# Kernel optimization log

Hardware: AMD Instinct MI355X
Metric: run time of the kernel (lower is better)

The kernel has to match this reference:

```python
import jax, jax.numpy as jnp
import numpy as np

NUM_HEADS = 8


def setup_inputs() -> dict:
    key = jax.random.key(0)
    ks = jax.random.split(key, 9)
    B, C, H, W = 2, 64, 48, 48
    Ck, Cv, Co = 64, 64, 64
    s = lambda fan_in: 1.0 / np.sqrt(fan_in)
    return {
        "x": jax.random.normal(ks[0], (B, C, H, W), jnp.float32),
        "Wq": jax.random.normal(ks[1], (Ck, C), jnp.float32) * s(C),
        "bq": jnp.zeros((Ck,), jnp.float32),
        "Wk": jax.random.normal(ks[2], (Ck, C), jnp.float32) * s(C),
        "bk": jnp.zeros((Ck,), jnp.float32),
        "Wv": jax.random.normal(ks[3], (Cv, C), jnp.float32) * s(C),
        "bv": jnp.zeros((Cv,), jnp.float32),
        "Wo": jax.random.normal(ks[4], (Co, Cv), jnp.float32) * s(Cv),
        "bo": jnp.zeros((Co,), jnp.float32),
    }


def _conv1x1(x, W, b):
    # 1x1 conv == channel matmul: [B,C,H,W] x [O,C] -> [B,O,H,W]
    return jnp.einsum("oc,bchw->bohw", W, x) + b[None, :, None, None]


def reference(x, Wq, bq, Wk, bk, Wv, bv, Wo, bo):
    B, _, H, W_ = x.shape
    nh = NUM_HEADS
    Ck, Cv = Wq.shape[0], Wv.shape[0]
    d = Ck // nh
    L = H * W_

    # NOTE: original torch code scales q in place via a view, so returned q is scaled.
    q = _conv1x1(x, Wq, bq) * (d ** -0.5)
    k = _conv1x1(x, Wk, bk)
    v = _conv1x1(x, Wv, bv)

    qs = q.reshape(B, nh, d, L)          # [B,h,d,Lq]
    ks = k.reshape(B, nh, d, L)          # [B,h,d,Lk]
    vs = v.reshape(B, nh, Cv // nh, L)   # [B,h,dv,Lk]

    logits = jnp.einsum("bhdq,bhdk->bhqk", qs, ks)   # [B,h,Lq,Lk]
    # softmax over the QUERY axis (dim=2), as in the original nn.Softmax(dim=2)
    weights = jax.nn.softmax(logits, axis=2)
    o = jnp.einsum("bhck,bhqk->bhcq", vs, weights)   # [B,h,dv,Lq]

    o = o.reshape(B, Cv, H, W_)
    out = _conv1x1(o, Wo, bo)
    return out, q
```

## Files before the change

kernel.cpp:

```cpp
#include <hip/hip_runtime.h>

#define LL   2304
#define CCH  64
#define NHD  8

static constexpr float QSCALE = 0.35355339059327373f;
static constexpr float LOG2E  = 1.4426950408889634f;

typedef _Float16 half2_t  __attribute__((ext_vector_type(2)));
typedef _Float16 half4_t  __attribute__((ext_vector_type(4)));
typedef _Float16 half8_t  __attribute__((ext_vector_type(8)));
typedef float    float16_t __attribute__((ext_vector_type(16)));

__device__ __forceinline__ half2_t pk_f16(float a, float b) {
    return __builtin_bit_cast(half2_t, __builtin_amdgcn_cvt_pkrtz(a, b));
}


__global__ __launch_bounds__(256) void k_qkv(
    const float* __restrict__ x,
    const float* __restrict__ Wq, const float* __restrict__ bq,
    const float* __restrict__ Wk, const float* __restrict__ bk,
    const float* __restrict__ Wv, const float* __restrict__ bv,
    const float* __restrict__ bo,
    float* __restrict__ qout, float* __restrict__ outp,
    _Float16* __restrict__ Qt, _Float16* __restrict__ Kt, _Float16* __restrict__ Vt)
{
    __shared__ float xs[64][32];
    __shared__ float wsm[64][64];
    const int t   = threadIdx.x;
    const int l0  = blockIdx.x * 32;
    const int b   = blockIdx.y;
    const int mat = blockIdx.z;
    const float* W    = (mat == 0) ? Wq : (mat == 1 ? Wk : Wv);
    const float* bias = (mat == 0) ? bq : (mat == 1 ? bk : bv);
    const float* xb = x + (long)b * CCH * LL;

    if (mat == 0) {
        #pragma unroll
        for (int p = 0; p < 2; ++p) {
            int flat = (p * 256 + t) * 4;
            int co = flat >> 5, l = flat & 31;
            float bv4 = bo[co];
            float4 vv = make_float4(bv4, bv4, bv4, bv4);
            *(float4*)&outp[((long)b * CCH + co) * LL + l0 + l] = vv;
        }
    }

    #pragma unroll
    for (int p = 0; p < 2; ++p) {
        int flat = (p * 256 + t) * 4;
        int c = flat >> 5, l = flat & 31;
        *(float4*)&xs[c][l] = *(const float4*)&xb[(long)c * LL + l0 + l];
    }
    #pragma unroll
    for (int p = 0; p < 4; ++p) {
        int flat = (p * 256 + t) * 4;
        int c = flat >> 6, l = flat & 63;
        *(float4*)&wsm[c][l] = *(const float4*)&W[flat];
    }
    __syncthreads();

    const int l  = t & 31;
    const int cg = t >> 5;
    float acc[8];
    #pragma unroll
    for (int j = 0; j < 8; ++j) acc[j] = 0.f;
    for (int cp = 0; cp < 64; ++cp) {
        float xv = xs[cp][l];
        #pragma unroll
        for (int j = 0; j < 8; ++j) acc[j] = fmaf(wsm[cg * 8 + j][cp], xv, acc[j]);
    }
    long row = (long)(b * NHD + cg) * LL + l0 + l;
    if (mat == 0) {
        half8_t pq;
        #pragma unroll
        for (int j = 0; j < 8; ++j) {
            float qv = (acc[j] + bias[cg * 8 + j]) * QSCALE;
            qout[((long)b * CCH + cg * 8 + j) * LL + l0 + l] = qv;
            pq[j] = (_Float16)(qv * LOG2E);
        }
        *(half8_t*)(Qt + row * 8) = pq;
    } else if (mat == 1) {
        half8_t pk;
        #pragma unroll
        for (int j = 0; j < 8; ++j) pk[j] = (_Float16)(acc[j] + bias[cg * 8 + j]);
        *(half8_t*)(Kt + row * 8) = pk;
    } else {
        half8_t pv;
        #pragma unroll
        for (int j = 0; j < 8; ++j) pv[j] = (_Float16)(acc[j] + bias[cg * 8 + j]);
        *(half8_t*)(Vt + row * 8) = pv;
    }
}

__global__ __launch_bounds__(256) void k_denom(
    const _Float16* __restrict__ Qt, const _Float16* __restrict__ Kt,
    const _Float16* __restrict__ Vt, _Float16* __restrict__ V2)
{
    __shared__ _Float16 lQ[2][256][4];
    __shared__ float Dp[4][32];
    __shared__ float rDs[32];
    const int t    = threadIdx.x;
    const int bh   = blockIdx.y;
    const int k0   = blockIdx.x * 32;
    const int lane = t & 63, w = t >> 6;
    const int half = lane >> 5, l31 = lane & 31;

    half4_t kA = *(const half4_t*)(Kt + ((long)bh * LL + k0 + l31) * 8 + half * 4);

    const float4* qbase = (const float4*)(Qt + (long)bh * LL * 8);
    float4 pre = qbase[t];

    float16_t Dacc = {};
    for (int ch = 0; ch < 9; ++ch) {
        __syncthreads();
        *(float2*)&lQ[0][t][0] = make_float2(pre.x, pre.y);
        *(float2*)&lQ[1][t][0] = make_float2(pre.z, pre.w);
        __syncthreads();
        if (ch + 1 < 9) pre = qbase[(ch + 1) * 256 + t];
        #pragma unroll
        for (int T = 0; T < 2; ++T) {
            half4_t qB = *(const half4_t*)&lQ[half][(2 * w + T) * 32 + l31][0];
            float16_t S = __builtin_amdgcn_mfma_f32_32x32x8f16(kA, qB, (float16_t){}, 0, 0, 0);
            #pragma unroll
            for (int r = 0; r < 16; ++r) Dacc[r] += __builtin_amdgcn_exp2f(S[r]);
        }
    }
    #pragma unroll
    for (int r = 0; r < 16; ++r) {
        float v = Dacc[r];
        v += __shfl_xor(v, 1);  v += __shfl_xor(v, 2);  v += __shfl_xor(v, 4);
        v += __shfl_xor(v, 8);  v += __shfl_xor(v, 16);
        Dacc[r] = v;
    }
    if (l31 == 0) {
        #pragma unroll
        for (int r = 0; r < 16; ++r) {
            int row = (r & 3) + 8 * (r >> 2) + 4 * half;
            Dp[w][row] = Dacc[r];
        }
    }
    __syncthreads();
    if (t < 32) rDs[t] = 256.0f / (Dp[0][t] + Dp[1][t] + Dp[2][t] + Dp[3][t]);
    __syncthreads();
    {
        int kk = t >> 3, c = t & 7;
        float v = (float)Vt[((long)bh * LL + k0 + kk) * 8 + c];
        V2[((long)bh * 8 + c) * LL + k0 + kk] = (_Float16)(v * rDs[kk]);
    }
}

__global__ __launch_bounds__(256, 4) void k_av_out(
    const _Float16* __restrict__ Qt, const _Float16* __restrict__ Kt,
    const _Float16* __restrict__ V2, const float* __restrict__ Wo,
    float* __restrict__ out)
{
    __shared__ _Float16 lK[2][64][4];
    __shared__ _Float16 lVt[8][72];
    __shared__ float WoT[64][68];
    const int t    = threadIdx.x;
    const int bh   = blockIdx.y;
    const int s    = blockIdx.z;
    const int b = bh >> 3, h = bh & 7;
    const int lane = t & 63, w = t >> 6;
    const int half = lane >> 5, l31 = lane & 31;
    const int q0   = blockIdx.x * 128 + w * 32;

    #pragma unroll
    for (int p = 0; p < 4; ++p) {
        int flat = p * 256 + t;
        int co = flat >> 4, cv4 = flat & 15;
        float4 v = *(const float4*)&Wo[co * 64 + cv4 * 4];
        WoT[cv4 * 4 + 0][co] = v.x; WoT[cv4 * 4 + 1][co] = v.y;
        WoT[cv4 * 4 + 2][co] = v.z; WoT[cv4 * 4 + 3][co] = v.w;
    }

    half4_t qB = *(const half4_t*)(Qt + ((long)bh * LL + q0 + l31) * 8 + half * 4);

    const long ks0 = (long)s * 576;
    const float4*    kbase = (const float4*)(Kt + ((long)bh * LL + ks0) * 8);
    const _Float16*  vbase = V2 + (long)bh * 8 * LL + ks0;

    float4 preK, preV;
    if (t < 64) preK = kbase[t];
    else if (t < 128) {
        int c = (t - 64) >> 3, j8 = (t - 64) & 7;
        preV = *(const float4*)(vbase + (long)c * LL + j8 * 8);
    }

    float16_t O = {};
    for (int ch = 0; ch < 9; ++ch) {
        __syncthreads();
        if (t < 64) {
            *(float2*)&lK[0][t][0] = make_float2(preK.x, preK.y);
            *(float2*)&lK[1][t][0] = make_float2(preK.z, preK.w);
        } else if (t < 128) {
            int c = (t - 64) >> 3, j8 = (t - 64) & 7;
            *(float4*)&lVt[c][j8 * 8] = preV;
        }
        __syncthreads();
        if (ch + 1 < 9) {
            if (t < 64) preK = kbase[(ch + 1) * 64 + t];
            else if (t < 128) {
                int c = (t - 64) >> 3, j8 = (t - 64) & 7;
                preV = *(const float4*)(vbase + (long)c * LL + (ch + 1) * 64 + j8 * 8);
            }
        }
        const int cl = l31 & 7;
        #pragma unroll
        for (int T = 0; T < 2; ++T) {
            int kb = T * 32;
            half4_t kA = *(const half4_t*)&lK[half][kb + l31][0];
            float16_t S = __builtin_amdgcn_mfma_f32_32x32x8f16(kA, qB, (float16_t){}, 0, 0, 0);
            #pragma unroll
            for (int g = 0; g < 4; ++g) {
                half2_t p0 = pk_f16(__builtin_amdgcn_exp2f(S[4 * g + 0]),
                                    __builtin_amdgcn_exp2f(S[4 * g + 1]));
                half2_t p1 = pk_f16(__builtin_amdgcn_exp2f(S[4 * g + 2]),
                                    __builtin_amdgcn_exp2f(S[4 * g + 3]));
                half4_t pB = __builtin_shufflevector(p0, p1, 0, 1, 2, 3);
                half4_t vA = *(const half4_t*)&lVt[cl][kb + g * 8 + half * 4];
                O = __builtin_amdgcn_mfma_f32_32x32x8f16(vA, pB, O, 0, 0, 0);
            }
        }
    }

    float ocl[4], och[4];
    #pragma unroll
    for (int r = 0; r < 4; ++r) {
        float mine  = O[r] * (1.0f / 256.0f);
        float other = __shfl_xor(mine, 32);
        ocl[r] = half ? other : mine;
        och[r] = half ? mine  : other;
    }
    float* ob = out + ((long)b * CCH) * LL + q0 + l31;
    #pragma unroll
    for (int g = 0; g < 2; ++g) {
        const int co0 = half * 32 + g * 16;
        float acc2[16];
        #pragma unroll
        for (int j = 0; j < 16; ++j) acc2[j] = 0.f;
        #pragma unroll
        for (int c = 0; c < 8; ++c) {
            float ov = (c < 4) ? ocl[c] : och[c - 4];
            #pragma unroll
            for (int j4 = 0; j4 < 4; ++j4) {
                const float4 wv = *(const float4*)&WoT[h * 8 + c][co0 + j4 * 4];
                acc2[j4 * 4 + 0] = fmaf(wv.x, ov, acc2[j4 * 4 + 0]);
                acc2[j4 * 4 + 1] = fmaf(wv.y, ov, acc2[j4 * 4 + 1]);
                acc2[j4 * 4 + 2] = fmaf(wv.z, ov, acc2[j4 * 4 + 2]);
                acc2[j4 * 4 + 3] = fmaf(wv.w, ov, acc2[j4 * 4 + 3]);
            }
        }
        #pragma unroll
        for (int j = 0; j < 16; ++j)
            atomicAdd(ob + (long)(co0 + j) * LL, acc2[j]);
    }
}

extern "C" void kernel_launch(void* const* d_in, const int* in_sizes, int n_in,
                              void* d_out, int out_size, void* d_ws, size_t ws_size,
                              hipStream_t stream)
{
    const float* x  = (const float*)d_in[0];
    const float* Wq = (const float*)d_in[1];
    const float* bq = (const float*)d_in[2];
    const float* Wk = (const float*)d_in[3];
    const float* bk = (const float*)d_in[4];
    const float* Wv = (const float*)d_in[5];
    const float* bv = (const float*)d_in[6];
    const float* Wo = (const float*)d_in[7];
    const float* bo = (const float*)d_in[8];

    float* out  = (float*)d_out;
    float* qout = out + 294912;

    _Float16* Qt = (_Float16*)d_ws;
    _Float16* Kt = Qt + 294912;
    _Float16* Vt = Kt + 294912;
    _Float16* V2 = Vt + 294912;

    k_qkv   <<<dim3(72, 2, 3),  256, 0, stream>>>(x, Wq, bq, Wk, bk, Wv, bv, bo,
                                                  qout, out, Qt, Kt, Vt);
    k_denom <<<dim3(72, 16),    256, 0, stream>>>(Qt, Kt, Vt, V2);
    k_av_out<<<dim3(18, 16, 4), 256, 0, stream>>>(Qt, Kt, V2, Wo, out);
}
```

Before: 127.3 us.

## Restructure attention-output kernel: all heads per block, 96 queries per wave, fewer atomics

The AV+output kernel now assigns one wave per head within a 512-thread block covering a 96-query tile, staging half of the key split (288 keys) for all heads in shared memory at once. Each wave reuses the staged K/V across three 32-query units. The per-head partial outputs are gathered in shared memory so the output projection sums over all 64 value channels before the atomic adds, cutting atomic traffic by the head count. The cost is much larger shared memory per block, the loss of the register prefetch double-buffering, and only 192 blocks in the grid, which may reduce occupancy and latency hiding.

```diff
diff --git a/kernel.cpp b/kernel.cpp
--- a/kernel.cpp
+++ b/kernel.cpp
@@ -151,111 +151,110 @@
     }
 }
 
-__global__ __launch_bounds__(256, 4) void k_av_out(
+__global__ __launch_bounds__(512) void k_av_out(
     const _Float16* __restrict__ Qt, const _Float16* __restrict__ Kt,
     const _Float16* __restrict__ V2, const float* __restrict__ Wo,
     float* __restrict__ out)
 {
-    __shared__ _Float16 lK[2][64][4];
-    __shared__ _Float16 lVt[8][72];
-    __shared__ float WoT[64][68];
+    __shared__ _Float16 lK[8][2][288][4];
+    __shared__ _Float16 lV[8][8][296];
+    __shared__ float    WoT[64][68];
+    __shared__ float    Os[64][100];
     const int t    = threadIdx.x;
-    const int bh   = blockIdx.y;
+    const int qb   = blockIdx.x;
+    const int b    = blockIdx.y;
     const int s    = blockIdx.z;
-    const int b = bh >> 3, h = bh & 7;
-    const int lane = t & 63, w = t >> 6;
+    const int lane = t & 63, h = t >> 6;
     const int half = lane >> 5, l31 = lane & 31;
-    const int q0   = blockIdx.x * 128 + w * 32;
-
-    #pragma unroll
-    for (int p = 0; p < 4; ++p) {
-        int flat = p * 256 + t;
+    const int cl   = l31 & 7;
+    const int bh   = b * NHD + h;
+
+    #pragma unroll
+    for (int p = 0; p < 2; ++p) {
+        int flat = p * 512 + t;
         int co = flat >> 4, cv4 = flat & 15;
         float4 v = *(const float4*)&Wo[co * 64 + cv4 * 4];
         WoT[cv4 * 4 + 0][co] = v.x; WoT[cv4 * 4 + 1][co] = v.y;
         WoT[cv4 * 4 + 2][co] = v.z; WoT[cv4 * 4 + 3][co] = v.w;
     }
 
-    half4_t qB = *(const half4_t*)(Qt + ((long)bh * LL + q0 + l31) * 8 + half * 4);
-
-    const long ks0 = (long)s * 576;
-    const float4*    kbase = (const float4*)(Kt + ((long)bh * LL + ks0) * 8);
-    const _Float16*  vbase = V2 + (long)bh * 8 * LL + ks0;
-
-    float4 preK, preV;
-    if (t < 64) preK = kbase[t];
-    else if (t < 128) {
-        int c = (t - 64) >> 3, j8 = (t - 64) & 7;
-        preV = *(const float4*)(vbase + (long)c * LL + j8 * 8);
-    }
-
-    float16_t O = {};
-    for (int ch = 0; ch < 9; ++ch) {
-        __syncthreads();
-        if (t < 64) {
-            *(float2*)&lK[0][t][0] = make_float2(preK.x, preK.y);
-            *(float2*)&lK[1][t][0] = make_float2(preK.z, preK.w);
-        } else if (t < 128) {
-            int c = (t - 64) >> 3, j8 = (t - 64) & 7;
-            *(float4*)&lVt[c][j8 * 8] = preV;
-        }
-        __syncthreads();
-        if (ch + 1 < 9) {
-            if (t < 64) preK = kbase[(ch + 1) * 64 + t];
-            else if (t < 128) {
-                int c = (t - 64) >> 3, j8 = (t - 64) & 7;
-                preV = *(const float4*)(vbase + (long)c * LL + (ch + 1) * 64 + j8 * 8);
-            }
-        }
-        const int cl = l31 & 7;
-        #pragma unroll
-        for (int T = 0; T < 2; ++T) {
-            int kb = T * 32;
-            half4_t kA = *(const half4_t*)&lK[half][kb + l31][0];
-            float16_t S = __builtin_amdgcn_mfma_f32_32x32x8f16(kA, qB, (float16_t){}, 0, 0, 0);
-            #pragma unroll
-            for (int g = 0; g < 4; ++g) {
-                half2_t p0 = pk_f16(__builtin_amdgcn_exp2f(S[4 * g + 0]),
-                                    __builtin_amdgcn_exp2f(S[4 * g + 1]));
-                half2_t p1 = pk_f16(__builtin_amdgcn_exp2f(S[4 * g + 2]),
-                                    __builtin_amdgcn_exp2f(S[4 * g + 3]));
-                half4_t pB = __builtin_shufflevector(p0, p1, 0, 1, 2, 3);
-                half4_t vA = *(const half4_t*)&lVt[cl][kb + g * 8 + half * 4];
-                O = __builtin_amdgcn_mfma_f32_32x32x8f16(vA, pB, O, 0, 0, 0);
-            }
-        }
-    }
-
-    float ocl[4], och[4];
+    const long qrow = (long)bh * LL + qb * 96 + l31;
+    half4_t qB0 = *(const half4_t*)(Qt + (qrow +  0) * 8 + half * 4);
+    half4_t qB1 = *(const half4_t*)(Qt + (qrow + 32) * 8 + half * 4);
+    half4_t qB2 = *(const half4_t*)(Qt + (qrow + 64) * 8 + half * 4);
+
+    float16_t O0 = {}, O1 = {}, O2 = {};
+
+    #define UNIT_STEP(Oacc, qBu)                                               \
+        _Pragma("unroll")                                                      \
+        for (int k32 = 0; k32 < 9; ++k32) {                                    \
+            const int kb = k32 * 32;                                           \
+            half4_t kA = *(const half4_t*)&lK[h][half][kb + l31][0];           \
+            float16_t S = __builtin_amdgcn_mfma_f32_32x32x8f16(kA, qBu, (float16_t){}, 0, 0, 0); \
+            _Pragma("unroll")                                                  \
+            for (int g = 0; g < 4; ++g) {                                      \
+                half2_t p0 = pk_f16(__builtin_amdgcn_exp2f(S[4*g+0]),          \
+                                    __builtin_amdgcn_exp2f(S[4*g+1]));         \
+                half2_t p1 = pk_f16(__builtin_amdgcn_exp2f(S[4*g+2]),          \
+                                    __builtin_amdgcn_exp2f(S[4*g+3]));         \
+                half4_t pB = __builtin_shufflevector(p0, p1, 0, 1, 2, 3);      \
+                half4_t vA = *(const half4_t*)&lV[h][cl][kb + g*8 + half*4];   \
+                Oacc = __builtin_amdgcn_mfma_f32_32x32x8f16(vA, pB, Oacc, 0, 0, 0); \
+            }                                                                  \
+        }
+
+    for (int kh = 0; kh < 2; ++kh) {
+        const long ksb = (long)s * 576 + kh * 288;
+        __syncthreads();
+        for (int i = t; i < 2304; i += 512) {
+            int hi = i / 288, row = i - hi * 288;
+            float4 kv = *(const float4*)&Kt[((long)(b * NHD + hi) * LL + ksb + row) * 8];
+            *(float2*)&lK[hi][0][row][0] = make_float2(kv.x, kv.y);
+            *(float2*)&lK[hi][1][row][0] = make_float2(kv.z, kv.w);
+        }
+        for (int i = t; i < 2304; i += 512) {
+            int r = i / 36, j = i - r * 36;
+            int hi = r >> 3, c = r & 7;
+            *(float4*)&lV[hi][c][j * 8] =
+                *(const float4*)&V2[((long)(b * NHD + hi) * NHD + c) * LL + ksb + j * 8];
+        }
+        __syncthreads();
+        UNIT_STEP(O0, qB0)
+        UNIT_STEP(O1, qB1)
+        UNIT_STEP(O2, qB2)
+    }
+    #undef UNIT_STEP
+
     #pragma unroll
     for (int r = 0; r < 4; ++r) {
-        float mine  = O[r] * (1.0f / 256.0f);
-        float other = __shfl_xor(mine, 32);
-        ocl[r] = half ? other : mine;
-        och[r] = half ? mine  : other;
-    }
-    float* ob = out + ((long)b * CCH) * LL + q0 + l31;
-    #pragma unroll
-    for (int g = 0; g < 2; ++g) {
-        const int co0 = half * 32 + g * 16;
-        float acc2[16];
-        #pragma unroll
-        for (int j = 0; j < 16; ++j) acc2[j] = 0.f;
-        #pragma unroll
-        for (int c = 0; c < 8; ++c) {
-            float ov = (c < 4) ? ocl[c] : och[c - 4];
+        const int c = r + 4 * half;
+        Os[h * 8 + c][ 0 + l31] = O0[r] * (1.0f / 256.0f);
+        Os[h * 8 + c][32 + l31] = O1[r] * (1.0f / 256.0f);
+        Os[h * 8 + c][64 + l31] = O2[r] * (1.0f / 256.0f);
+    }
+    __syncthreads();
+
+    if (t < 384) {
+        const int q   = t % 96;
+        const int cog = t / 96;
+        float acc[16];
+        #pragma unroll
+        for (int j = 0; j < 16; ++j) acc[j] = 0.f;
+        for (int cv = 0; cv < 64; ++cv) {
+            float ov = Os[cv][q];
             #pragma unroll
             for (int j4 = 0; j4 < 4; ++j4) {
-                const float4 wv = *(const float4*)&WoT[h * 8 + c][co0 + j4 * 4];
-                acc2[j4 * 4 + 0] = fmaf(wv.x, ov, acc2[j4 * 4 + 0]);
-                acc2[j4 * 4 + 1] = fmaf(wv.y, ov, acc2[j4 * 4 + 1]);
-                acc2[j4 * 4 + 2] = fmaf(wv.z, ov, acc2[j4 * 4 + 2]);
-                acc2[j4 * 4 + 3] = fmaf(wv.w, ov, acc2[j4 * 4 + 3]);
+                float4 wv = *(const float4*)&WoT[cv][cog * 16 + j4 * 4];
+                acc[j4 * 4 + 0] = fmaf(wv.x, ov, acc[j4 * 4 + 0]);
+                acc[j4 * 4 + 1] = fmaf(wv.y, ov, acc[j4 * 4 + 1]);
+                acc[j4 * 4 + 2] = fmaf(wv.z, ov, acc[j4 * 4 + 2]);
+                acc[j4 * 4 + 3] = fmaf(wv.w, ov, acc[j4 * 4 + 3]);
             }
         }
+        float* ob = out + ((long)b * CCH + cog * 16) * LL + qb * 96 + q;
         #pragma unroll
         for (int j = 0; j < 16; ++j)
-            atomicAdd(ob + (long)(co0 + j) * LL, acc2[j]);
+            atomicAdd(ob + (long)j * LL, acc[j]);
     }
 }
 
@@ -281,8 +280,8 @@
     _Float16* Vt = Kt + 294912;
     _Float16* V2 = Vt + 294912;
 
-    k_qkv   <<<dim3(72, 2, 3),  256, 0, stream>>>(x, Wq, bq, Wk, bk, Wv, bv, bo,
-                                                  qout, out, Qt, Kt, Vt);
-    k_denom <<<dim3(72, 16),    256, 0, stream>>>(Qt, Kt, Vt, V2);
-    k_av_out<<<dim3(18, 16, 4), 256, 0, stream>>>(Qt, Kt, V2, Wo, out);
-}
+    k_qkv   <<<dim3(72, 2, 3), 256, 0, stream>>>(x, Wq, bq, Wk, bk, Wv, bv, bo,
+                                                 qout, out, Qt, Kt, Vt);
+    k_denom <<<dim3(72, 16),   256, 0, stream>>>(Qt, Kt, Vt, V2);
+    k_av_out<<<dim3(24, 2, 4), 512, 0, stream>>>(Qt, Kt, V2, Wo, out);
+}
```

Result: faster. 116.5 us (-8.5%).

## Split key range across warps within block and reduce partials in LDS before output projection

Applied to the files above, without the earlier changes.

The attention-output kernel now gives each block 32 queries, and its four warps each cover a quarter of the key range, instead of four warps covering different query tiles with the key range split across grid z-blocks. Per-warp partial outputs are summed through shared memory before a single output projection, so fewer atomic adds reach global memory. Only the head's 8-column slice of Wo is staged, replacing the full transpose. This increases per-block LDS staging traffic and adds a barrier-based reduction at the end.

```diff
diff --git a/kernel.cpp b/kernel.cpp
--- a/kernel.cpp
+++ b/kernel.cpp
@@ -156,62 +156,50 @@
     const _Float16* __restrict__ V2, const float* __restrict__ Wo,
     float* __restrict__ out)
 {
-    __shared__ _Float16 lK[2][64][4];
-    __shared__ _Float16 lVt[8][72];
-    __shared__ float WoT[64][68];
+    __shared__ _Float16 lK[4][2][64][4];
+    __shared__ _Float16 lV[4][8][72];
+    __shared__ float    WoS[64][9];
+    __shared__ float    Osp[4][8][33];
     const int t    = threadIdx.x;
+    const int qb   = blockIdx.x;
     const int bh   = blockIdx.y;
-    const int s    = blockIdx.z;
     const int b = bh >> 3, h = bh & 7;
     const int lane = t & 63, w = t >> 6;
     const int half = lane >> 5, l31 = lane & 31;
-    const int q0   = blockIdx.x * 128 + w * 32;
-
-    #pragma unroll
-    for (int p = 0; p < 4; ++p) {
-        int flat = p * 256 + t;
-        int co = flat >> 4, cv4 = flat & 15;
-        float4 v = *(const float4*)&Wo[co * 64 + cv4 * 4];
-        WoT[cv4 * 4 + 0][co] = v.x; WoT[cv4 * 4 + 1][co] = v.y;
-        WoT[cv4 * 4 + 2][co] = v.z; WoT[cv4 * 4 + 3][co] = v.w;
-    }
-
-    half4_t qB = *(const half4_t*)(Qt + ((long)bh * LL + q0 + l31) * 8 + half * 4);
-
-    const long ks0 = (long)s * 576;
-    const float4*    kbase = (const float4*)(Kt + ((long)bh * LL + ks0) * 8);
-    const _Float16*  vbase = V2 + (long)bh * 8 * LL + ks0;
-
-    float4 preK, preV;
-    if (t < 64) preK = kbase[t];
-    else if (t < 128) {
-        int c = (t - 64) >> 3, j8 = (t - 64) & 7;
-        preV = *(const float4*)(vbase + (long)c * LL + j8 * 8);
-    }
+    const int cl   = l31 & 7;
+
+    if (t < 128) {
+        int co = t >> 1, c4 = (t & 1) * 4;
+        float4 v = *(const float4*)&Wo[co * 64 + h * 8 + c4];
+        WoS[co][c4 + 0] = v.x; WoS[co][c4 + 1] = v.y;
+        WoS[co][c4 + 2] = v.z; WoS[co][c4 + 3] = v.w;
+    }
+
+    half4_t qB = *(const half4_t*)(Qt + ((long)bh * LL + qb * 32 + l31) * 8 + half * 4);
+
+    const int sw = t >> 6, sr = t & 63;
+    const int vc = (t & 63) >> 3, vj = t & 7;
+    const _Float16* kbg = Kt + ((long)bh * LL + 576 * sw) * 8;
+    const _Float16* vbg = V2 + ((long)bh * 8 + vc) * LL + 576 * sw + vj * 8;
+
+    float4 preK = *(const float4*)(kbg + (long)sr * 8);
+    float4 preV = *(const float4*)(vbg);
 
     float16_t O = {};
-    for (int ch = 0; ch < 9; ++ch) {
-        __syncthreads();
-        if (t < 64) {
-            *(float2*)&lK[0][t][0] = make_float2(preK.x, preK.y);
-            *(float2*)&lK[1][t][0] = make_float2(preK.z, preK.w);
-        } else if (t < 128) {
-            int c = (t - 64) >> 3, j8 = (t - 64) & 7;
-            *(float4*)&lVt[c][j8 * 8] = preV;
-        }
-        __syncthreads();
-        if (ch + 1 < 9) {
-            if (t < 64) preK = kbase[(ch + 1) * 64 + t];
-            else if (t < 128) {
-                int c = (t - 64) >> 3, j8 = (t - 64) & 7;
-                preV = *(const float4*)(vbase + (long)c * LL + (ch + 1) * 64 + j8 * 8);
-            }
-        }
-        const int cl = l31 & 7;
+    for (int it = 0; it < 9; ++it) {
+        __syncthreads();
+        *(float2*)&lK[sw][0][sr][0] = make_float2(preK.x, preK.y);
+        *(float2*)&lK[sw][1][sr][0] = make_float2(preK.z, preK.w);
+        *(float4*)&lV[sw][vc][vj * 8] = preV;
+        __syncthreads();
+        if (it + 1 < 9) {
+            preK = *(const float4*)(kbg + (long)(64 * (it + 1) + sr) * 8);
+            preV = *(const float4*)(vbg + 64 * (it + 1));
+        }
         #pragma unroll
         for (int T = 0; T < 2; ++T) {
-            int kb = T * 32;
-            half4_t kA = *(const half4_t*)&lK[half][kb + l31][0];
+            const int kb = T * 32;
+            half4_t kA = *(const half4_t*)&lK[w][half][kb + l31][0];
             float16_t S = __builtin_amdgcn_mfma_f32_32x32x8f16(kA, qB, (float16_t){}, 0, 0, 0);
             #pragma unroll
             for (int g = 0; g < 4; ++g) {
@@ -220,42 +208,32 @@
                 half2_t p1 = pk_f16(__builtin_amdgcn_exp2f(S[4 * g + 2]),
                                     __builtin_amdgcn_exp2f(S[4 * g + 3]));
                 half4_t pB = __builtin_shufflevector(p0, p1, 0, 1, 2, 3);
-                half4_t vA = *(const half4_t*)&lVt[cl][kb + g * 8 + half * 4];
+                half4_t vA = *(const half4_t*)&lV[w][cl][kb + g * 8 + half * 4];
                 O = __builtin_amdgcn_mfma_f32_32x32x8f16(vA, pB, O, 0, 0, 0);
             }
         }
     }
 
-    float ocl[4], och[4];
-    #pragma unroll
-    for (int r = 0; r < 4; ++r) {
-        float mine  = O[r] * (1.0f / 256.0f);
-        float other = __shfl_xor(mine, 32);
-        ocl[r] = half ? other : mine;
-        och[r] = half ? mine  : other;
-    }
-    float* ob = out + ((long)b * CCH) * LL + q0 + l31;
-    #pragma unroll
-    for (int g = 0; g < 2; ++g) {
-        const int co0 = half * 32 + g * 16;
-        float acc2[16];
-        #pragma unroll
-        for (int j = 0; j < 16; ++j) acc2[j] = 0.f;
-        #pragma unroll
-        for (int c = 0; c < 8; ++c) {
-            float ov = (c < 4) ? ocl[c] : och[c - 4];
+    #pragma unroll
+    for (int r = 0; r < 4; ++r)
+        Osp[w][r + 4 * half][l31] = O[r] * (1.0f / 256.0f);
+    __syncthreads();
+
+    {
+        const int q = t & 31, cog = t >> 5;
+        float o8[8];
+        #pragma unroll
+        for (int c = 0; c < 8; ++c)
+            o8[c] = Osp[0][c][q] + Osp[1][c][q] + Osp[2][c][q] + Osp[3][c][q];
+        float* ob = out + ((long)b * CCH + cog * 8) * LL + qb * 32 + q;
+        #pragma unroll
+        for (int j = 0; j < 8; ++j) {
+            float a = 0.f;
             #pragma unroll
-            for (int j4 = 0; j4 < 4; ++j4) {
-                const float4 wv = *(const float4*)&WoT[h * 8 + c][co0 + j4 * 4];
-                acc2[j4 * 4 + 0] = fmaf(wv.x, ov, acc2[j4 * 4 + 0]);
-                acc2[j4 * 4 + 1] = fmaf(wv.y, ov, acc2[j4 * 4 + 1]);
-                acc2[j4 * 4 + 2] = fmaf(wv.z, ov, acc2[j4 * 4 + 2]);
-                acc2[j4 * 4 + 3] = fmaf(wv.w, ov, acc2[j4 * 4 + 3]);
-            }
-        }
-        #pragma unroll
-        for (int j = 0; j < 16; ++j)
-            atomicAdd(ob + (long)(co0 + j) * LL, acc2[j]);
+            for (int c = 0; c < 8; ++c)
+                a = fmaf(WoS[cog * 8 + j][c], o8[c], a);
+            atomicAdd(ob + (long)j * LL, a);
+        }
     }
 }
 
@@ -281,8 +259,8 @@
     _Float16* Vt = Kt + 294912;
     _Float16* V2 = Vt + 294912;
 
-    k_qkv   <<<dim3(72, 2, 3),  256, 0, stream>>>(x, Wq, bq, Wk, bk, Wv, bv, bo,
-                                                  qout, out, Qt, Kt, Vt);
-    k_denom <<<dim3(72, 16),    256, 0, stream>>>(Qt, Kt, Vt, V2);
-    k_av_out<<<dim3(18, 16, 4), 256, 0, stream>>>(Qt, Kt, V2, Wo, out);
-}
+    k_qkv   <<<dim3(72, 2, 3), 256, 0, stream>>>(x, Wq, bq, Wk, bk, Wv, bv, bo,
+                                                 qout, out, Qt, Kt, Vt);
+    k_denom <<<dim3(72, 16),   256, 0, stream>>>(Qt, Kt, Vt, V2);
+    k_av_out<<<dim3(72, 16),   256, 0, stream>>>(Qt, Kt, V2, Wo, out);
+}
```

Measured after the change: 106.5 us. 16.4% less time.
